# Performance work log

Hardware: AMD Instinct MI355X
Metric: run time of the kernel (lower is better)

Reference implementation:

```python
import jax, jax.numpy as jnp
import numpy as np

C = 64
NUM_GROUPS = 16  # per Normalize() logic for in_channels=64
EPS = 1e-5

def group_norm(x, gamma, beta):
    b, c, h, w, d = x.shape
    xg = x.reshape(b, NUM_GROUPS, c // NUM_GROUPS, h, w, d)
    mean = xg.mean(axis=(2, 3, 4, 5), keepdims=True)
    var = xg.var(axis=(2, 3, 4, 5), keepdims=True)
    xg = (xg - mean) * jax.lax.rsqrt(var + EPS)
    xn = xg.reshape(b, c, h, w, d)
    return xn * gamma[None, :, None, None, None] + beta[None, :, None, None, None]

def conv1x1(x, w, b):
    # 1x1x1 conv3d == channel mixing: w is [out_c, in_c]
    return jnp.einsum('bchwd,oc->bohwd', x, w) + b[None, :, None, None, None]

def setup_inputs() -> dict:
    key = jax.random.key(0)
    ks = jax.random.split(key, 11)
    s = 1.0 / np.sqrt(C)
    return {
        'x': jax.random.normal(ks[0], (2, C, 16, 16, 16), dtype=jnp.float32),
        'norm_w': jnp.ones((C,), jnp.float32),
        'norm_b': jnp.zeros((C,), jnp.float32),
        'q_w': jax.random.uniform(ks[1], (C, C), jnp.float32, -s, s),
        'q_b': jax.random.uniform(ks[2], (C,), jnp.float32, -s, s),
        'k_w': jax.random.uniform(ks[3], (C, C), jnp.float32, -s, s),
        'k_b': jax.random.uniform(ks[4], (C,), jnp.float32, -s, s),
        'v_w': jax.random.uniform(ks[5], (C, C), jnp.float32, -s, s),
        'v_b': jax.random.uniform(ks[6], (C,), jnp.float32, -s, s),
        'proj_w': jax.random.uniform(ks[7], (C, C), jnp.float32, -s, s),
        'proj_b': jax.random.uniform(ks[8], (C,), jnp.float32, -s, s),
    }

def reference(x, norm_w, norm_b, q_w, q_b, k_w, k_b, v_w, v_b, proj_w, proj_b):
    b, c, h, w, d = x.shape
    n = h * w * d
    hn = group_norm(x, norm_w, norm_b)
    q = conv1x1(hn, q_w, q_b).reshape(b, c, n)   # [b, c, n]
    k = conv1x1(hn, k_w, k_b).reshape(b, c, n)
    v = conv1x1(hn, v_w, v_b).reshape(b, c, n)
    scale = c ** (-0.5)
    scores = jnp.einsum('bcq,bck->bqk', q, k) * scale   # [b, n_q, n_k]
    attn = jax.nn.softmax(scores, axis=2)
    out = jnp.einsum('bck,bqk->bcq', v, attn)            # [b, c, n]
    out = out.reshape(b, c, h, w, d)
    out = conv1x1(out, proj_w, proj_b)
    return x + out
```

## Files before the change

### kernel.cpp

```cpp
#include <hip/hip_runtime.h>
#include <hip/hip_bf16.h>

#define B 2
#define C 64
#define N 4096
#define EPS 1e-5f
#define QSCALE_LOG2E 0.18033688f

using short8 = __attribute__((ext_vector_type(8))) short;
using f32x16 = __attribute__((ext_vector_type(16))) float;

__device__ inline short f2bf(float f) {
  __hip_bfloat16 h = __float2bfloat16(f);
  union { __hip_bfloat16 h; short s; } u; u.h = h; return u.s;
}
__device__ inline float bf2f(short s) {
  union { unsigned u; float f; } u;
  u.u = ((unsigned)(unsigned short)s) << 16;
  return u.f;
}
__device__ inline int packbf(float a, float b) {
  return (int)((unsigned short)f2bf(a) | ((unsigned)(unsigned short)f2bf(b) << 16));
}

__global__ __launch_bounds__(256) void gn_stats_kernel(
    const float* __restrict__ x, const float* __restrict__ gw,
    const float* __restrict__ gb, float* __restrict__ ascale,
    float* __restrict__ bshift) {
  int bg = blockIdx.x;
  int b = bg >> 4, g = bg & 15;
  const float4* xv = (const float4*)(x + (size_t)(b * C + g * 4) * N);
  int tid = threadIdx.x;

  float s = 0.f, s2 = 0.f;
  for (int i = tid; i < N; i += 256) {
    float4 v = xv[i];
    s += v.x + v.y + v.z + v.w;
    s2 += v.x * v.x + v.y * v.y + v.z * v.z + v.w * v.w;
  }
  __shared__ float ss[256], ss2[256];
  ss[tid] = s; ss2[tid] = s2;
  __syncthreads();
  for (int st = 128; st > 0; st >>= 1) {
    if (tid < st) { ss[tid] += ss[tid + st]; ss2[tid] += ss2[tid + st]; }
    __syncthreads();
  }
  if (tid < 4) {
    float mean = ss[0] * (1.f / (4 * N));
    float var = ss2[0] * (1.f / (4 * N)) - mean * mean;
    float inv = rsqrtf(var + EPS);
    int c = g * 4 + tid;
    float a = inv * gw[c];
    ascale[b * C + c] = a;
    bshift[b * C + c] = gb[c] - mean * a;
  }
}

__global__ __launch_bounds__(256) void qkv_kernel(
    const float* __restrict__ x, const float* __restrict__ ascale,
    const float* __restrict__ bshift,
    const float* __restrict__ qw, const float* __restrict__ qb,
    const float* __restrict__ kw, const float* __restrict__ kb,
    const float* __restrict__ vw, const float* __restrict__ vb,
    short* __restrict__ q_t, short* __restrict__ k_t, short* __restrict__ v_b) {
  int o0 = blockIdx.y * 4, b = blockIdx.z;
  int pos = blockIdx.x * 256 + threadIdx.x;
  const float* xp = x + (size_t)b * C * N + pos;
  const float* as = ascale + b * C;
  const float* bs = bshift + b * C;

  float sq[4] = {0.f, 0.f, 0.f, 0.f};
  float sk[4] = {0.f, 0.f, 0.f, 0.f};
  float sv[4] = {0.f, 0.f, 0.f, 0.f};
#pragma unroll
  for (int c = 0; c < C; ++c) {
    float hv = fmaf(xp[(size_t)c * N], as[c], bs[c]);
#pragma unroll
    for (int j = 0; j < 4; ++j) {
      sq[j] = fmaf(qw[(o0 + j) * C + c], hv, sq[j]);
      sk[j] = fmaf(kw[(o0 + j) * C + c], hv, sk[j]);
      sv[j] = fmaf(vw[(o0 + j) * C + c], hv, sv[j]);
    }
  }
  size_t ti = ((size_t)b * N + pos) * C;
  short4 qv, kv;
  qv.x = f2bf((sq[0] + qb[o0 + 0]) * QSCALE_LOG2E);
  qv.y = f2bf((sq[1] + qb[o0 + 1]) * QSCALE_LOG2E);
  qv.z = f2bf((sq[2] + qb[o0 + 2]) * QSCALE_LOG2E);
  qv.w = f2bf((sq[3] + qb[o0 + 3]) * QSCALE_LOG2E);
  kv.x = f2bf(sk[0] + kb[o0 + 0]);
  kv.y = f2bf(sk[1] + kb[o0 + 1]);
  kv.z = f2bf(sk[2] + kb[o0 + 2]);
  kv.w = f2bf(sk[3] + kb[o0 + 3]);
  *(short4*)&q_t[ti + o0] = qv;
  *(short4*)&k_t[ti + o0] = kv;
#pragma unroll
  for (int j = 0; j < 4; ++j)
    v_b[((size_t)b * C + o0 + j) * N + pos] = f2bf(sv[j] + vb[o0 + j]);
}

__global__ __launch_bounds__(256) void attn_kernel(
    const short* __restrict__ q_t, const short* __restrict__ k_t,
    const short* __restrict__ v_b, short* __restrict__ opart,
    float* __restrict__ lpart, int segLen, int kseg) {
  int b = blockIdx.z, s = blockIdx.y;
  int l = threadIdx.x & 63;
  int q0 = blockIdx.x * 256 + (threadIdx.x >> 6) * 64;
  int lo5 = l & 31;
  int hi = l >> 5;

  const short* qp = q_t + (size_t)b * N * C;
  const short* kp = k_t + (size_t)b * N * C;
  const short* vp = v_b + (size_t)b * C * N;

  short8 qf[2][4];
#pragma unroll
  for (int qt = 0; qt < 2; ++qt)
#pragma unroll
    for (int t = 0; t < 4; ++t)
      qf[qt][t] = *(const short8*)&qp[(size_t)(q0 + qt * 32 + lo5) * C + t * 16 + hi * 8];

  f32x16 oacc00, oacc01, oacc10, oacc11;
#pragma unroll
  for (int i = 0; i < 16; ++i) { oacc00[i] = 0.f; oacc01[i] = 0.f; oacc10[i] = 0.f; oacc11[i] = 0.f; }
  float lsum[2] = {0.f, 0.f};

  int kbase = s * segLen;
  for (int kc = 0; kc < segLen; kc += 32) {
    int k0 = kbase + kc;
    short8 kf[4];
#pragma unroll
    for (int t = 0; t < 4; ++t)
      kf[t] = *(const short8*)&kp[(size_t)(k0 + lo5) * C + t * 16 + hi * 8];

    f32x16 sacc[2];
#pragma unroll
    for (int i = 0; i < 16; ++i) { sacc[0][i] = 0.f; sacc[1][i] = 0.f; }
#pragma unroll
    for (int t = 0; t < 4; ++t) {
      sacc[0] = __builtin_amdgcn_mfma_f32_32x32x16_bf16(kf[t], qf[0][t], sacc[0], 0, 0, 0);
      sacc[1] = __builtin_amdgcn_mfma_f32_32x32x16_bf16(kf[t], qf[1][t], sacc[1], 0, 0, 0);
    }

    short8 pfrag[2][2];
#pragma unroll
    for (int qt = 0; qt < 2; ++qt) {
      float ps = 0.f;
#pragma unroll
      for (int i = 0; i < 16; ++i) { sacc[qt][i] = exp2f(sacc[qt][i]); ps += sacc[qt][i]; }
      lsum[qt] += ps;

      union U { int i[4]; short8 v; } f0, f1;
      {
        int x0 = packbf(sacc[qt][0], sacc[qt][1]), z0 = packbf(sacc[qt][2], sacc[qt][3]);
        int y0 = packbf(sacc[qt][4], sacc[qt][5]), w0 = packbf(sacc[qt][6], sacc[qt][7]);
        int xs = __shfl_xor(x0, 32), zs = __shfl_xor(z0, 32);
        int ys = __shfl_xor(y0, 32), ws2 = __shfl_xor(w0, 32);
        f0.i[0] = hi ? ys : x0; f0.i[1] = hi ? ws2 : z0;
        f0.i[2] = hi ? y0 : xs; f0.i[3] = hi ? w0 : zs;
      }
      {
        int x0 = packbf(sacc[qt][8], sacc[qt][9]), z0 = packbf(sacc[qt][10], sacc[qt][11]);
        int y0 = packbf(sacc[qt][12], sacc[qt][13]), w0 = packbf(sacc[qt][14], sacc[qt][15]);
        int xs = __shfl_xor(x0, 32), zs = __shfl_xor(z0, 32);
        int ys = __shfl_xor(y0, 32), ws2 = __shfl_xor(w0, 32);
        f1.i[0] = hi ? ys : x0; f1.i[1] = hi ? ws2 : z0;
        f1.i[2] = hi ? y0 : xs; f1.i[3] = hi ? w0 : zs;
      }
      pfrag[qt][0] = f0.v;
      pfrag[qt][1] = f1.v;
    }

#pragma unroll
    for (int mm = 0; mm < 2; ++mm) {
      short8 vf0 = *(const short8*)&vp[(size_t)(lo5) * N + k0 + mm * 16 + hi * 8];
      short8 vf1 = *(const short8*)&vp[(size_t)(32 + lo5) * N + k0 + mm * 16 + hi * 8];
      oacc00 = __builtin_amdgcn_mfma_f32_32x32x16_bf16(vf0, pfrag[0][mm], oacc00, 0, 0, 0);
      oacc01 = __builtin_amdgcn_mfma_f32_32x32x16_bf16(vf1, pfrag[0][mm], oacc01, 0, 0, 0);
      oacc10 = __builtin_amdgcn_mfma_f32_32x32x16_bf16(vf0, pfrag[1][mm], oacc10, 0, 0, 0);
      oacc11 = __builtin_amdgcn_mfma_f32_32x32x16_bf16(vf1, pfrag[1][mm], oacc11, 0, 0, 0);
    }
  }

#pragma unroll
  for (int qt = 0; qt < 2; ++qt) {
    lsum[qt] += __shfl_xor(lsum[qt], 32);
    int qq = q0 + qt * 32 + lo5;
    short* op = opart + (size_t)(b * kseg + s) * C * N;
#pragma unroll
    for (int r = 0; r < 16; ++r) {
      int c = (r & 3) + 8 * (r >> 2) + 4 * hi;
      float v0 = (qt == 0) ? oacc00[r] : oacc10[r];
      float v1 = (qt == 0) ? oacc01[r] : oacc11[r];
      op[(size_t)c * N + qq] = f2bf(v0);
      op[(size_t)(c + 32) * N + qq] = f2bf(v1);
    }
    if (hi == 0) lpart[(size_t)(b * kseg + s) * N + qq] = lsum[qt];
  }
}

__global__ __launch_bounds__(256) void merge_kernel(
    const short* __restrict__ opart, const float* __restrict__ lpart,
    short* __restrict__ attnout, int kseg) {
  int idx = blockIdx.x * 256 + threadIdx.x;
  int q4 = (idx & 1023) * 4;
  int c = (idx >> 10) & 63;
  int b = idx >> 16;

  float o[4] = {0.f, 0.f, 0.f, 0.f};
  float L[4] = {0.f, 0.f, 0.f, 0.f};
  for (int s = 0; s < kseg; ++s) {
    float4 lv = *(const float4*)&lpart[(size_t)(b * kseg + s) * N + q4];
    L[0] += lv.x; L[1] += lv.y; L[2] += lv.z; L[3] += lv.w;
    short4 ov = *(const short4*)&opart[((size_t)(b * kseg + s) * C + c) * N + q4];
    o[0] += bf2f(ov.x); o[1] += bf2f(ov.y); o[2] += bf2f(ov.z); o[3] += bf2f(ov.w);
  }
  short4 r;
  r.x = f2bf(o[0] / L[0]); r.y = f2bf(o[1] / L[1]);
  r.z = f2bf(o[2] / L[2]); r.w = f2bf(o[3] / L[3]);
  *(short4*)&attnout[(size_t)(b * C + c) * N + q4] = r;
}

__global__ __launch_bounds__(256) void proj_kernel(
    const short* __restrict__ at, const float* __restrict__ pw,
    const float* __restrict__ pb, const float* __restrict__ x,
    float* __restrict__ out) {
  int o0 = blockIdx.y * 4, b = blockIdx.z;
  int pos = blockIdx.x * 256 + threadIdx.x;
  const short* h = at + (size_t)b * C * N + pos;
  float sum[4] = {0.f, 0.f, 0.f, 0.f};
#pragma unroll
  for (int c = 0; c < C; ++c) {
    float hv = bf2f(h[(size_t)c * N]);
#pragma unroll
    for (int j = 0; j < 4; ++j) sum[j] = fmaf(pw[(o0 + j) * C + c], hv, sum[j]);
  }
#pragma unroll
  for (int j = 0; j < 4; ++j) {
    size_t oi = (size_t)(b * C + o0 + j) * N + pos;
    out[oi] = x[oi] + sum[j] + pb[o0 + j];
  }
}

extern "C" void kernel_launch(void* const* d_in, const int* in_sizes, int n_in,
                              void* d_out, int out_size, void* d_ws, size_t ws_size,
                              hipStream_t stream) {
  const float* x      = (const float*)d_in[0];
  const float* norm_w = (const float*)d_in[1];
  const float* norm_b = (const float*)d_in[2];
  const float* q_w    = (const float*)d_in[3];
  const float* q_b    = (const float*)d_in[4];
  const float* k_w    = (const float*)d_in[5];
  const float* k_b    = (const float*)d_in[6];
  const float* v_w    = (const float*)d_in[7];
  const float* v_b    = (const float*)d_in[8];
  const float* proj_w = (const float*)d_in[9];
  const float* proj_b = (const float*)d_in[10];
  float* out = (float*)d_out;

  const size_t BCN = (size_t)B * C * N;

  int kseg = 16;
  auto need = [&](int s) -> size_t {
    return BCN * 2 * 4
         + (2 * B * C + (size_t)s * B * N) * 4
         + (size_t)s * BCN * 2;
  };
  while (kseg > 1 && need(kseg) > ws_size) kseg >>= 1;
  int segLen = N / kseg;

  short* q_t    = (short*)d_ws;
  short* k_t    = q_t + BCN;
  short* vbuf   = k_t + BCN;
  short* attnout = vbuf + BCN;
  float* ascale = (float*)(attnout + BCN);
  float* bshift = ascale + B * C;
  float* lpart  = bshift + B * C;
  short* opart  = (short*)(lpart + (size_t)kseg * B * N);

  gn_stats_kernel<<<B * 16, 256, 0, stream>>>(x, norm_w, norm_b, ascale, bshift);

  qkv_kernel<<<dim3(N / 256, C / 4, B), 256, 0, stream>>>(
      x, ascale, bshift, q_w, q_b, k_w, k_b, v_w, v_b, q_t, k_t, vbuf);

  attn_kernel<<<dim3(N / 256, kseg, B), 256, 0, stream>>>(
      q_t, k_t, vbuf, opart, lpart, segLen, kseg);

  merge_kernel<<<(int)(BCN / 4 / 256), 256, 0, stream>>>(
      opart, lpart, attnout, kseg);

  proj_kernel<<<dim3(N / 256, C / 4, B), 256, 0, stream>>>(
      attnout, proj_w, proj_b, x, out);
}
```

Measured before the change: 66.26 us.

## Split groupnorm stats, widen qkv/proj tiles, double-buffer attention K/V loads

Group-norm statistics now use a two-stage reduction: 512 blocks compute partial sums and a tiny kernel finalizes scale and shift, replacing 32 long serial blocks. The qkv and proj kernels now compute 8 output channels per thread instead of 4, so each x or attn load is reused more and q/k stores become 16-byte. The attention loop is software-pipelined with double-buffered K/V register fragments and s_setprio hints around the MFMA sections, so global loads overlap compute. The cost is an extra launch, higher register pressure, and fewer blocks in the qkv and proj kernels.

```diff
diff --git a/kernel.cpp b/kernel.cpp
--- a/kernel.cpp
+++ b/kernel.cpp
@@ -23,21 +23,15 @@
   return (int)((unsigned short)f2bf(a) | ((unsigned)(unsigned short)f2bf(b) << 16));
 }
 
-__global__ __launch_bounds__(256) void gn_stats_kernel(
-    const float* __restrict__ x, const float* __restrict__ gw,
-    const float* __restrict__ gb, float* __restrict__ ascale,
-    float* __restrict__ bshift) {
-  int bg = blockIdx.x;
-  int b = bg >> 4, g = bg & 15;
-  const float4* xv = (const float4*)(x + (size_t)(b * C + g * 4) * N);
+__global__ __launch_bounds__(256) void gn_part_kernel(
+    const float* __restrict__ x, float2* __restrict__ part) {
+  int blk = blockIdx.x;
+  int bg = blk >> 4, sl = blk & 15;
+  const float4* xv = (const float4*)(x + (size_t)bg * 4 * N) + sl * 256;
   int tid = threadIdx.x;
-
-  float s = 0.f, s2 = 0.f;
-  for (int i = tid; i < N; i += 256) {
-    float4 v = xv[i];
-    s += v.x + v.y + v.z + v.w;
-    s2 += v.x * v.x + v.y * v.y + v.z * v.z + v.w * v.w;
-  }
+  float4 v = xv[tid];
+  float s = v.x + v.y + v.z + v.w;
+  float s2 = v.x * v.x + v.y * v.y + v.z * v.z + v.w * v.w;
   __shared__ float ss[256], ss2[256];
   ss[tid] = s; ss2[tid] = s2;
   __syncthreads();
@@ -45,15 +39,28 @@
     if (tid < st) { ss[tid] += ss[tid + st]; ss2[tid] += ss2[tid + st]; }
     __syncthreads();
   }
-  if (tid < 4) {
-    float mean = ss[0] * (1.f / (4 * N));
-    float var = ss2[0] * (1.f / (4 * N)) - mean * mean;
-    float inv = rsqrtf(var + EPS);
-    int c = g * 4 + tid;
-    float a = inv * gw[c];
-    ascale[b * C + c] = a;
-    bshift[b * C + c] = gb[c] - mean * a;
-  }
+  if (tid == 0) part[blk] = make_float2(ss[0], ss2[0]);
+}
+
+__global__ __launch_bounds__(128) void gn_final_kernel(
+    const float2* __restrict__ part, const float* __restrict__ gw,
+    const float* __restrict__ gb, float* __restrict__ ascale,
+    float* __restrict__ bshift) {
+  int t = threadIdx.x;
+  int c = t & 63, b = t >> 6, g = c >> 2;
+  int bg = b * 16 + g;
+  float s = 0.f, s2 = 0.f;
+#pragma unroll
+  for (int sl = 0; sl < 16; ++sl) {
+    float2 p = part[bg * 16 + sl];
+    s += p.x; s2 += p.y;
+  }
+  float mean = s * (1.f / 16384.f);
+  float var = s2 * (1.f / 16384.f) - mean * mean;
+  float inv = rsqrtf(var + EPS);
+  float a = inv * gw[c];
+  ascale[t] = a;
+  bshift[t] = gb[c] - mean * a;
 }
 
 __global__ __launch_bounds__(256) void qkv_kernel(
@@ -63,40 +70,63 @@
     const float* __restrict__ kw, const float* __restrict__ kb,
     const float* __restrict__ vw, const float* __restrict__ vb,
     short* __restrict__ q_t, short* __restrict__ k_t, short* __restrict__ v_b) {
-  int o0 = blockIdx.y * 4, b = blockIdx.z;
+  int o0 = blockIdx.y * 8, b = blockIdx.z;
   int pos = blockIdx.x * 256 + threadIdx.x;
   const float* xp = x + (size_t)b * C * N + pos;
   const float* as = ascale + b * C;
   const float* bs = bshift + b * C;
 
-  float sq[4] = {0.f, 0.f, 0.f, 0.f};
-  float sk[4] = {0.f, 0.f, 0.f, 0.f};
-  float sv[4] = {0.f, 0.f, 0.f, 0.f};
+  float sq[8], sk[8], sv[8];
+#pragma unroll
+  for (int j = 0; j < 8; ++j) { sq[j] = 0.f; sk[j] = 0.f; sv[j] = 0.f; }
 #pragma unroll
   for (int c = 0; c < C; ++c) {
     float hv = fmaf(xp[(size_t)c * N], as[c], bs[c]);
 #pragma unroll
-    for (int j = 0; j < 4; ++j) {
+    for (int j = 0; j < 8; ++j) {
       sq[j] = fmaf(qw[(o0 + j) * C + c], hv, sq[j]);
       sk[j] = fmaf(kw[(o0 + j) * C + c], hv, sk[j]);
       sv[j] = fmaf(vw[(o0 + j) * C + c], hv, sv[j]);
     }
   }
   size_t ti = ((size_t)b * N + pos) * C;
-  short4 qv, kv;
-  qv.x = f2bf((sq[0] + qb[o0 + 0]) * QSCALE_LOG2E);
-  qv.y = f2bf((sq[1] + qb[o0 + 1]) * QSCALE_LOG2E);
-  qv.z = f2bf((sq[2] + qb[o0 + 2]) * QSCALE_LOG2E);
-  qv.w = f2bf((sq[3] + qb[o0 + 3]) * QSCALE_LOG2E);
-  kv.x = f2bf(sk[0] + kb[o0 + 0]);
-  kv.y = f2bf(sk[1] + kb[o0 + 1]);
-  kv.z = f2bf(sk[2] + kb[o0 + 2]);
-  kv.w = f2bf(sk[3] + kb[o0 + 3]);
-  *(short4*)&q_t[ti + o0] = qv;
-  *(short4*)&k_t[ti + o0] = kv;
-#pragma unroll
-  for (int j = 0; j < 4; ++j)
+  short8 qv, kv;
+#pragma unroll
+  for (int j = 0; j < 8; ++j) {
+    qv[j] = f2bf((sq[j] + qb[o0 + j]) * QSCALE_LOG2E);
+    kv[j] = f2bf(sk[j] + kb[o0 + j]);
+  }
+  *(short8*)&q_t[ti + o0] = qv;
+  *(short8*)&k_t[ti + o0] = kv;
+#pragma unroll
+  for (int j = 0; j < 8; ++j)
     v_b[((size_t)b * C + o0 + j) * N + pos] = f2bf(sv[j] + vb[o0 + j]);
+}
+
+__device__ inline void softpack(f32x16& s, int hi, float& lsum,
+                                short8& p0, short8& p1) {
+  float ps = 0.f;
+#pragma unroll
+  for (int i = 0; i < 16; ++i) { s[i] = exp2f(s[i]); ps += s[i]; }
+  lsum += ps;
+  union U { int i[4]; short8 v; } f0, f1;
+  {
+    int x0 = packbf(s[0], s[1]), z0 = packbf(s[2], s[3]);
+    int y0 = packbf(s[4], s[5]), w0 = packbf(s[6], s[7]);
+    int xs = __shfl_xor(x0, 32), zs = __shfl_xor(z0, 32);
+    int ys = __shfl_xor(y0, 32), ws2 = __shfl_xor(w0, 32);
+    f0.i[0] = hi ? ys : x0; f0.i[1] = hi ? ws2 : z0;
+    f0.i[2] = hi ? y0 : xs; f0.i[3] = hi ? w0 : zs;
+  }
+  {
+    int x0 = packbf(s[8], s[9]), z0 = packbf(s[10], s[11]);
+    int y0 = packbf(s[12], s[13]), w0 = packbf(s[14], s[15]);
+    int xs = __shfl_xor(x0, 32), zs = __shfl_xor(z0, 32);
+    int ys = __shfl_xor(y0, 32), ws2 = __shfl_xor(w0, 32);
+    f1.i[0] = hi ? ys : x0; f1.i[1] = hi ? ws2 : z0;
+    f1.i[2] = hi ? y0 : xs; f1.i[3] = hi ? w0 : zs;
+  }
+  p0 = f0.v; p1 = f1.v;
 }
 
 __global__ __launch_bounds__(256) void attn_kernel(
@@ -126,60 +156,54 @@
   float lsum[2] = {0.f, 0.f};
 
   int kbase = s * segLen;
-  for (int kc = 0; kc < segLen; kc += 32) {
-    int k0 = kbase + kc;
-    short8 kf[4];
-#pragma unroll
-    for (int t = 0; t < 4; ++t)
-      kf[t] = *(const short8*)&kp[(size_t)(k0 + lo5) * C + t * 16 + hi * 8];
-
-    f32x16 sacc[2];
-#pragma unroll
-    for (int i = 0; i < 16; ++i) { sacc[0][i] = 0.f; sacc[1][i] = 0.f; }
-#pragma unroll
-    for (int t = 0; t < 4; ++t) {
-      sacc[0] = __builtin_amdgcn_mfma_f32_32x32x16_bf16(kf[t], qf[0][t], sacc[0], 0, 0, 0);
-      sacc[1] = __builtin_amdgcn_mfma_f32_32x32x16_bf16(kf[t], qf[1][t], sacc[1], 0, 0, 0);
-    }
-
-    short8 pfrag[2][2];
-#pragma unroll
-    for (int qt = 0; qt < 2; ++qt) {
-      float ps = 0.f;
-#pragma unroll
-      for (int i = 0; i < 16; ++i) { sacc[qt][i] = exp2f(sacc[qt][i]); ps += sacc[qt][i]; }
-      lsum[qt] += ps;
-
-      union U { int i[4]; short8 v; } f0, f1;
-      {
-        int x0 = packbf(sacc[qt][0], sacc[qt][1]), z0 = packbf(sacc[qt][2], sacc[qt][3]);
-        int y0 = packbf(sacc[qt][4], sacc[qt][5]), w0 = packbf(sacc[qt][6], sacc[qt][7]);
-        int xs = __shfl_xor(x0, 32), zs = __shfl_xor(z0, 32);
-        int ys = __shfl_xor(y0, 32), ws2 = __shfl_xor(w0, 32);
-        f0.i[0] = hi ? ys : x0; f0.i[1] = hi ? ws2 : z0;
-        f0.i[2] = hi ? y0 : xs; f0.i[3] = hi ? w0 : zs;
-      }
-      {
-        int x0 = packbf(sacc[qt][8], sacc[qt][9]), z0 = packbf(sacc[qt][10], sacc[qt][11]);
-        int y0 = packbf(sacc[qt][12], sacc[qt][13]), w0 = packbf(sacc[qt][14], sacc[qt][15]);
-        int xs = __shfl_xor(x0, 32), zs = __shfl_xor(z0, 32);
-        int ys = __shfl_xor(y0, 32), ws2 = __shfl_xor(w0, 32);
-        f1.i[0] = hi ? ys : x0; f1.i[1] = hi ? ws2 : z0;
-        f1.i[2] = hi ? y0 : xs; f1.i[3] = hi ? w0 : zs;
-      }
-      pfrag[qt][0] = f0.v;
-      pfrag[qt][1] = f1.v;
-    }
-
-#pragma unroll
-    for (int mm = 0; mm < 2; ++mm) {
-      short8 vf0 = *(const short8*)&vp[(size_t)(lo5) * N + k0 + mm * 16 + hi * 8];
-      short8 vf1 = *(const short8*)&vp[(size_t)(32 + lo5) * N + k0 + mm * 16 + hi * 8];
-      oacc00 = __builtin_amdgcn_mfma_f32_32x32x16_bf16(vf0, pfrag[0][mm], oacc00, 0, 0, 0);
-      oacc01 = __builtin_amdgcn_mfma_f32_32x32x16_bf16(vf1, pfrag[0][mm], oacc01, 0, 0, 0);
-      oacc10 = __builtin_amdgcn_mfma_f32_32x32x16_bf16(vf0, pfrag[1][mm], oacc10, 0, 0, 0);
-      oacc11 = __builtin_amdgcn_mfma_f32_32x32x16_bf16(vf1, pfrag[1][mm], oacc11, 0, 0, 0);
-    }
+
+#define LOAD_KF(DST, K0)                                                     \
+  _Pragma("unroll") for (int t = 0; t < 4; ++t)                              \
+      DST[t] = *(const short8*)&kp[(size_t)((K0) + lo5) * C + t * 16 + hi * 8];
+#define LOAD_VF(DST, K0)                                                     \
+  DST[0] = *(const short8*)&vp[(size_t)(lo5) * N + (K0) + hi * 8];           \
+  DST[1] = *(const short8*)&vp[(size_t)(32 + lo5) * N + (K0) + hi * 8];      \
+  DST[2] = *(const short8*)&vp[(size_t)(lo5) * N + (K0) + 16 + hi * 8];      \
+  DST[3] = *(const short8*)&vp[(size_t)(32 + lo5) * N + (K0) + 16 + hi * 8];
+
+#define CHUNK(KF, VF)                                                        \
+  {                                                                          \
+    f32x16 s0_, s1_;                                                         \
+    _Pragma("unroll") for (int i = 0; i < 16; ++i) { s0_[i] = 0.f; s1_[i] = 0.f; } \
+    __builtin_amdgcn_s_setprio(1);                                           \
+    _Pragma("unroll") for (int t = 0; t < 4; ++t) {                          \
+      s0_ = __builtin_amdgcn_mfma_f32_32x32x16_bf16(KF[t], qf[0][t], s0_, 0, 0, 0); \
+      s1_ = __builtin_amdgcn_mfma_f32_32x32x16_bf16(KF[t], qf[1][t], s1_, 0, 0, 0); \
+    }                                                                        \
+    __builtin_amdgcn_s_setprio(0);                                           \
+    short8 pf00, pf01, pf10, pf11;                                           \
+    softpack(s0_, hi, lsum[0], pf00, pf01);                                  \
+    softpack(s1_, hi, lsum[1], pf10, pf11);                                  \
+    __builtin_amdgcn_s_setprio(1);                                           \
+    oacc00 = __builtin_amdgcn_mfma_f32_32x32x16_bf16(VF[0], pf00, oacc00, 0, 0, 0); \
+    oacc01 = __builtin_amdgcn_mfma_f32_32x32x16_bf16(VF[1], pf00, oacc01, 0, 0, 0); \
+    oacc10 = __builtin_amdgcn_mfma_f32_32x32x16_bf16(VF[0], pf10, oacc10, 0, 0, 0); \
+    oacc11 = __builtin_amdgcn_mfma_f32_32x32x16_bf16(VF[1], pf10, oacc11, 0, 0, 0); \
+    oacc00 = __builtin_amdgcn_mfma_f32_32x32x16_bf16(VF[2], pf01, oacc00, 0, 0, 0); \
+    oacc01 = __builtin_amdgcn_mfma_f32_32x32x16_bf16(VF[3], pf01, oacc01, 0, 0, 0); \
+    oacc10 = __builtin_amdgcn_mfma_f32_32x32x16_bf16(VF[2], pf11, oacc10, 0, 0, 0); \
+    oacc11 = __builtin_amdgcn_mfma_f32_32x32x16_bf16(VF[3], pf11, oacc11, 0, 0, 0); \
+    __builtin_amdgcn_s_setprio(0);                                           \
+  }
+
+  short8 kf0[4], kf1[4], vf0[4], vf1[4];
+  LOAD_KF(kf0, kbase)
+  LOAD_VF(vf0, kbase)
+
+  for (int kc = 0; kc < segLen; kc += 64) {
+    int kA = kbase + kc;
+    LOAD_KF(kf1, kA + 32)
+    LOAD_VF(vf1, kA + 32)
+    CHUNK(kf0, vf0)
+    int kN = (kc + 64 < segLen) ? (kA + 64) : kA;
+    LOAD_KF(kf0, kN)
+    LOAD_VF(vf0, kN)
+    CHUNK(kf1, vf1)
   }
 
 #pragma unroll
@@ -197,6 +221,9 @@
     }
     if (hi == 0) lpart[(size_t)(b * kseg + s) * N + qq] = lsum[qt];
   }
+#undef LOAD_KF
+#undef LOAD_VF
+#undef CHUNK
 }
 
 __global__ __launch_bounds__(256) void merge_kernel(
@@ -225,18 +252,20 @@
     const short* __restrict__ at, const float* __restrict__ pw,
     const float* __restrict__ pb, const float* __restrict__ x,
     float* __restrict__ out) {
-  int o0 = blockIdx.y * 4, b = blockIdx.z;
+  int o0 = blockIdx.y * 8, b = blockIdx.z;
   int pos = blockIdx.x * 256 + threadIdx.x;
   const short* h = at + (size_t)b * C * N + pos;
-  float sum[4] = {0.f, 0.f, 0.f, 0.f};
+  float sum[8];
+#pragma unroll
+  for (int j = 0; j < 8; ++j) sum[j] = 0.f;
 #pragma unroll
   for (int c = 0; c < C; ++c) {
     float hv = bf2f(h[(size_t)c * N]);
 #pragma unroll
-    for (int j = 0; j < 4; ++j) sum[j] = fmaf(pw[(o0 + j) * C + c], hv, sum[j]);
-  }
-#pragma unroll
-  for (int j = 0; j < 4; ++j) {
+    for (int j = 0; j < 8; ++j) sum[j] = fmaf(pw[(o0 + j) * C + c], hv, sum[j]);
+  }
+#pragma unroll
+  for (int j = 0; j < 8; ++j) {
     size_t oi = (size_t)(b * C + o0 + j) * N + pos;
     out[oi] = x[oi] + sum[j] + pb[o0 + j];
   }
@@ -263,24 +292,26 @@
   int kseg = 16;
   auto need = [&](int s) -> size_t {
     return BCN * 2 * 4
-         + (2 * B * C + (size_t)s * B * N) * 4
+         + (2 * B * C + 1024 + (size_t)s * B * N) * 4
          + (size_t)s * BCN * 2;
   };
   while (kseg > 1 && need(kseg) > ws_size) kseg >>= 1;
   int segLen = N / kseg;
 
-  short* q_t    = (short*)d_ws;
-  short* k_t    = q_t + BCN;
-  short* vbuf   = k_t + BCN;
+  short* q_t     = (short*)d_ws;
+  short* k_t     = q_t + BCN;
+  short* vbuf    = k_t + BCN;
   short* attnout = vbuf + BCN;
-  float* ascale = (float*)(attnout + BCN);
-  float* bshift = ascale + B * C;
-  float* lpart  = bshift + B * C;
-  short* opart  = (short*)(lpart + (size_t)kseg * B * N);
-
-  gn_stats_kernel<<<B * 16, 256, 0, stream>>>(x, norm_w, norm_b, ascale, bshift);
-
-  qkv_kernel<<<dim3(N / 256, C / 4, B), 256, 0, stream>>>(
+  float* ascale  = (float*)(attnout + BCN);
+  float* bshift  = ascale + B * C;
+  float2* part   = (float2*)(bshift + B * C);
+  float* lpart   = (float*)(part + 512);
+  short* opart   = (short*)(lpart + (size_t)kseg * B * N);
+
+  gn_part_kernel<<<512, 256, 0, stream>>>(x, part);
+  gn_final_kernel<<<1, 128, 0, stream>>>(part, norm_w, norm_b, ascale, bshift);
+
+  qkv_kernel<<<dim3(N / 256, C / 8, B), 256, 0, stream>>>(
       x, ascale, bshift, q_w, q_b, k_w, k_b, v_w, v_b, q_t, k_t, vbuf);
 
   attn_kernel<<<dim3(N / 256, kseg, B), 256, 0, stream>>>(
@@ -289,6 +320,6 @@
   merge_kernel<<<(int)(BCN / 4 / 256), 256, 0, stream>>>(
       opart, lpart, attnout, kseg);
 
-  proj_kernel<<<dim3(N / 256, C / 4, B), 256, 0, stream>>>(
+  proj_kernel<<<dim3(N / 256, C / 8, B), 256, 0, stream>>>(
       attnout, proj_w, proj_b, x, out);
 }
```

Result: slower. 77.09 us (+16.3%).
